# Kernel tuning notes

Hardware: AMD Instinct MI355X
Metric: run time of the kernel (lower is better)

## Reference

```python
import jax, jax.numpy as jnp
import numpy as np

J, H, MAXREL = 24, 8, 49  # num_joints, temporal heads, max_relative_position


def _pos_encoding(seq_len, d_model):
    pos = jnp.arange(seq_len, dtype=jnp.float32)[:, None]
    i = jnp.arange(d_model, dtype=jnp.float32)[None, :]
    angle = pos / jnp.power(10000.0, 2.0 * jnp.floor(i / 2.0) / d_model)
    return jnp.where(jnp.arange(d_model)[None, :] % 2 == 0, jnp.sin(angle), jnp.cos(angle))  # [S, D]


def _rel_index(seq_len):
    r = jnp.arange(seq_len)
    dist = jnp.clip(r[None, :] - r[:, None], -MAXREL, MAXREL) + MAXREL
    return dist  # [S, S] int


def setup_inputs() -> dict:
    key = jax.random.key(0)
    ks = jax.random.split(key, 12)
    B, S, D = 32, 120, 128
    depth = D // H
    s = 0.02
    x = jax.random.normal(ks[0], (B, S, J, D), dtype=jnp.float32)
    mask = jnp.triu(jnp.ones((1, 1, S, S), dtype=jnp.float32), k=1)  # look-ahead mask
    Wq = jax.random.normal(ks[1], (J, D, D), dtype=jnp.float32) * s
    bq = jnp.zeros((J, D), dtype=jnp.float32)
    Wk = jax.random.normal(ks[2], (J, D, D), dtype=jnp.float32) * s
    bk = jnp.zeros((J, D), dtype=jnp.float32)
    Wv = jax.random.normal(ks[3], (J, D, D), dtype=jnp.float32) * s
    bv = jnp.zeros((J, D), dtype=jnp.float32)
    Wo = jax.random.normal(ks[4], (D, D), dtype=jnp.float32) * s
    bo = jnp.zeros((D,), dtype=jnp.float32)
    key_table = jax.random.normal(ks[5], (2 * MAXREL + 1, depth), dtype=jnp.float32) * s
    val_table = jax.random.normal(ks[6], (2 * MAXREL + 1, depth), dtype=jnp.float32) * s
    return {"x": x, "mask": mask, "Wq": Wq, "bq": bq, "Wk": Wk, "bk": bk,
            "Wv": Wv, "bv": bv, "Wo": Wo, "bo": bo,
            "key_table": key_table, "val_table": val_table}


def reference(x, mask, Wq, bq, Wk, bk, Wv, bv, Wo, bo, key_table, val_table):
    B, S, _, D = x.shape
    depth = D // H
    # absolute positional encoding, broadcast over batch and joints
    x = x + _pos_encoding(S, D)[None, :, None, :]
    xj = jnp.transpose(x, (2, 0, 1, 3))  # [J, B, S, D]
    # per-joint linear projections (torch Linear: y = x @ W^T + b)
    q = jnp.einsum('jbsd,jed->jbse', xj, Wq) + bq[:, None, None, :]
    k = jnp.einsum('jbsd,jed->jbse', xj, Wk) + bk[:, None, None, :]
    v = jnp.einsum('jbsd,jed->jbse', xj, Wv) + bv[:, None, None, :]
    # split heads -> [J, B, H, S, depth]
    split = lambda t: t.reshape(J, B, S, H, depth).transpose(0, 1, 3, 2, 4)
    q, k, v = split(q), split(k), split(v)
    # relative key/value embeddings [S, S, depth]
    rel = _rel_index(S)
    rk = key_table[rel]
    rv = val_table[rel]
    logits = jnp.einsum('jbhsd,jbhtd->jbhst', q, k) + jnp.einsum('jbhsd,std->jbhst', q, rk)
    logits = logits / jnp.float32(np.sqrt(depth)) + mask * (-1e9)
    w = jax.nn.softmax(logits, axis=-1)  # [J, B, H, S, T]
    out = jnp.einsum('jbhst,jbhtd->jbhsd', w, v) + jnp.einsum('jbhst,std->jbhsd', w, rv)
    out = out.transpose(0, 1, 3, 2, 4).reshape(J, B, S, D)  # merge heads
    out = jnp.einsum('jbsd,ed->jbse', out, Wo) + bo  # shared output projection
    outputs = out.transpose(1, 2, 0, 3)  # [B, S, J, D]
    attn_weights = w[..., -1, :].transpose(1, 0, 2, 3)  # [B, J, H, T]
    return outputs, attn_weights
```

## Files before the change

kernel.cpp:

```cpp
#include <hip/hip_runtime.h>
#include <math.h>

#define Jn 24
#define Bn 32
#define Sn 120
#define Dn 128
#define Hn 8
#define DEP 16
#define ALD 136

#define QSCL 0.36067376022224085f

typedef short bf16x8 __attribute__((ext_vector_type(8)));
typedef float f32x4 __attribute__((ext_vector_type(4)));

#if __has_builtin(__builtin_amdgcn_exp2f)
#define EXP2(x) __builtin_amdgcn_exp2f(x)
#else
#define EXP2(x) exp2f(x)
#endif

__device__ __forceinline__ unsigned short f2b(float f) {
    union { float f; unsigned u; } v; v.f = f;
    unsigned r = v.u + 0x7FFFu + ((v.u >> 16) & 1u);
    return (unsigned short)(r >> 16);
}
__device__ __forceinline__ float b2f(unsigned u16) {
    union { unsigned u; float f; } v; v.u = u16 << 16;
    return v.f;
}

__global__ void pe_kernel(float* __restrict__ pe) {
    const int s = blockIdx.x, d = threadIdx.x;
    const float expo = (float)(2 * (d >> 1)) / (float)Dn;
    const float base = powf(10000.0f, -expo);
    const float ang = (float)s * base;
    pe[s * Dn + d] = (d & 1) ? cosf(ang) : sinf(ang);
}

__global__ __launch_bounds__(256)
void qkv_gemm(const float* __restrict__ x, const float* __restrict__ pe,
              const float* __restrict__ Wq, const float* __restrict__ bq,
              const float* __restrict__ Wk, const float* __restrict__ bk,
              const float* __restrict__ Wv, const float* __restrict__ bv,
              unsigned short* __restrict__ qg, unsigned short* __restrict__ kg,
              unsigned short* __restrict__ vg, int jbase)
{
    extern __shared__ unsigned short lsu[];
    unsigned short* As = lsu;
    unsigned short* Bs = lsu + 128 * ALD;

    const int bid = blockIdx.x;
    const int mt = bid % 30;
    const int jc = bid / 30;
    const int j = jbase + jc;
    const int tid = threadIdx.x;

    for (int idx = tid; idx < 128 * 32; idx += 256) {
        const int r = idx >> 5;
        const int c = (idx & 31) << 2;
        const int mflat = mt * 128 + r;
        const int b = mflat / Sn;
        const int s = mflat % Sn;
        const float4 xv = *(const float4*)(x + (((size_t)(b * Sn + s)) * Jn + j) * Dn + c);
        const float4 pv = *(const float4*)(pe + s * Dn + c);
        unsigned short* dst = As + r * ALD + c;
        dst[0] = f2b(xv.x + pv.x); dst[1] = f2b(xv.y + pv.y);
        dst[2] = f2b(xv.z + pv.z); dst[3] = f2b(xv.w + pv.w);
    }

    const int wid = tid >> 6;
    const int lane = tid & 63;
    const int wm = wid >> 1, wn = wid & 1;
    const int g = lane >> 4, q16 = lane & 15;

    for (int nt = 0; nt < 3; ++nt) {
        const float* Wsel = (nt == 0 ? Wq : (nt == 1 ? Wk : Wv)) + (size_t)j * Dn * Dn;
        const float* bsel = (nt == 0 ? bq : (nt == 1 ? bk : bv)) + (size_t)j * Dn;
        unsigned short* obuf = (nt == 0 ? qg : (nt == 1 ? kg : vg));
        const float scl = (nt == 0) ? QSCL : 1.0f;

        if (nt) __syncthreads();
        for (int idx = tid; idx < 128 * 32; idx += 256) {
            const int e = idx >> 5;
            const int c = (idx & 31) << 2;
            const float4 wv = *(const float4*)(Wsel + (size_t)e * Dn + c);
            unsigned short* dst = Bs + e * ALD + c;
            dst[0] = f2b(wv.x); dst[1] = f2b(wv.y); dst[2] = f2b(wv.z); dst[3] = f2b(wv.w);
        }
        __syncthreads();

        f32x4 acc[4][4];
        #pragma unroll
        for (int a = 0; a < 4; ++a)
            #pragma unroll
            for (int c2 = 0; c2 < 4; ++c2) acc[a][c2] = (f32x4){0.f, 0.f, 0.f, 0.f};

        #pragma unroll
        for (int ks = 0; ks < 4; ++ks) {
            const int kof = ks * 32 + g * 8;
            bf16x8 av[4], bvf[4];
            #pragma unroll
            for (int fr = 0; fr < 4; ++fr)
                av[fr] = *(const bf16x8*)(As + (wm * 64 + fr * 16 + q16) * ALD + kof);
            #pragma unroll
            for (int fc = 0; fc < 4; ++fc)
                bvf[fc] = *(const bf16x8*)(Bs + (wn * 64 + fc * 16 + q16) * ALD + kof);
            #pragma unroll
            for (int fr = 0; fr < 4; ++fr)
                #pragma unroll
                for (int fc = 0; fc < 4; ++fc)
                    acc[fr][fc] = __builtin_amdgcn_mfma_f32_16x16x32_bf16(av[fr], bvf[fc], acc[fr][fc], 0, 0, 0);
        }

        #pragma unroll
        for (int fc = 0; fc < 4; ++fc) {
            const int e = wn * 64 + fc * 16 + q16;
            const float be = bsel[e];
            const int h = e >> 4, ed = e & 15;
            #pragma unroll
            for (int fr = 0; fr < 4; ++fr) {
                #pragma unroll
                for (int r = 0; r < 4; ++r) {
                    const int mflat = mt * 128 + wm * 64 + fr * 16 + g * 4 + r;
                    const int b = mflat / Sn, s = mflat % Sn;
                    obuf[((size_t)((jc * Bn + b) * Hn + h)) * (Sn * DEP) + s * DEP + ed] =
                        f2b((acc[fr][fc][r] + be) * scl);
                }
            }
        }
    }
}

#define AB_LD  184
#define A_VCT  0
#define A_RKT  5888
#define A_RV0  8384
#define A_ABUF 8448
#define A_QRB  32000
#define A_BYTES 40448

__global__ __launch_bounds__(256)
void attn_mfma(const unsigned short* __restrict__ qg, const unsigned short* __restrict__ kg,
               const unsigned short* __restrict__ vg,
               const float* __restrict__ ktab, const float* __restrict__ vtab,
               unsigned short* __restrict__ out_pre, float* __restrict__ attn_w, int jbase)
{
    extern __shared__ char smc[];
    unsigned short* vct = (unsigned short*)(smc + A_VCT);
    unsigned short* rkt = (unsigned short*)(smc + A_RKT);
    float*          rv0 = (float*)(smc + A_RV0);

    const int tid = threadIdx.x;
    const int wid = tid >> 6;
    const int lane = tid & 63;
    const int l15 = lane & 15;
    const int g = lane >> 4;
    const int bh = blockIdx.x;
    const int jc = bh >> 8;
    const int b = (bh >> 3) & 31;
    const int h = bh & 7;
    const int j = jbase + jc;

    unsigned short* ab = (unsigned short*)(smc + A_ABUF) + wid * 16 * AB_LD;
    _Float16*      qrb = (_Float16*)(smc + A_QRB) + wid * 16 * 66;

    {
        unsigned* z = (unsigned*)smc;
        for (int idx = tid; idx < A_BYTES / 4; idx += 256) z[idx] = 0;
    }
    __syncthreads();
    const unsigned* vs = (const unsigned*)vg + (size_t)bh * 960;
    for (int idx = tid; idx < 960; idx += 256) {
        const int s = idx >> 3, ep = idx & 7;
        const unsigned u = vs[idx];
        vct[(2 * ep) * AB_LD + s] = (unsigned short)(u & 0xffffu);
        vct[(2 * ep + 1) * AB_LD + s] = (unsigned short)(u >> 16);
    }
    for (int idx = tid; idx < 800; idx += 256) {
        const int d = idx >> 4, e = idx & 15;
        vct[e * AB_LD + 120 + d] = f2b(vtab[d * DEP + e] - vtab[e]);
    }
    for (int idx = tid; idx < 800; idx += 256) {
        const int d = idx >> 4, e = idx & 15;
        rkt[d * 24 + e] = f2b(ktab[d * DEP + e]);
    }
    if (tid < 16) rv0[tid] = vtab[tid];
    __syncthreads();

    const unsigned short* qgu = qg + (size_t)bh * 1920;
    const unsigned short* kgu = kg + (size_t)bh * 1920;

    const bf16x8 zf = {0, 0, 0, 0, 0, 0, 0, 0};
    const f32x4 z4 = {0.f, 0.f, 0.f, 0.f};
    const float rv0f = rv0[l15];

    #pragma unroll
    for (int half = 0; half < 2; ++half) {
        const int m = half ? (7 - wid) : wid;

        const bf16x8 afr = (g < 2) ? *(const bf16x8*)(qgu + (16 * m + l15) * 16 + g * 8) : zf;
        f32x4 qr[4];
        #pragma unroll
        for (int n = 0; n < 4; ++n) {
            const bf16x8 bfr = (g < 2) ? *(const bf16x8*)(rkt + (16 * n + l15) * 24 + g * 8) : zf;
            qr[n] = __builtin_amdgcn_mfma_f32_16x16x32_bf16(afr, bfr, z4, 0, 0, 0);
        }
        f32x4 acc[8];
        #pragma unroll
        for (int n = 0; n < 8; ++n) {
            if (n > m) break;
            const bf16x8 bfr = (g < 2) ? *(const bf16x8*)(kgu + (16 * n + l15) * 16 + g * 8) : zf;
            acc[n] = __builtin_amdgcn_mfma_f32_16x16x32_bf16(afr, bfr, z4, 0, 0, 0);
        }
        #pragma unroll
        for (int n = 0; n < 4; ++n)
            #pragma unroll
            for (int r = 0; r < 4; ++r)
                qrb[(g * 4 + r) * 66 + 16 * n + l15] = (_Float16)qr[n][r];

        float rs[4];
        #pragma unroll
        for (int r = 0; r < 4; ++r) {
            const int srow = 16 * m + g * 4 + r;
            float pv[8];
            float tot = 0.f;
            #pragma unroll
            for (int n = 0; n < 8; ++n) {
                if (n > m) break;
                const int t = 16 * n + l15;
                const int dd = t - srow;
                int dist = dd + 49;
                dist = dist < 0 ? 0 : (dist > 49 ? 49 : dist);
                const float qrv = (float)qrb[(g * 4 + r) * 66 + dist];
                float p = 0.f;
                if (t <= srow) p = EXP2(acc[n][r] + qrv);
                pv[n] = p;
                tot += p;
            }
            #pragma unroll
            for (int mk = 1; mk < 16; mk <<= 1) tot += __shfl_xor(tot, mk);
            rs[r] = tot;
            #pragma unroll
            for (int n = 0; n < 8; ++n) {
                if (n > m) break;
                const int t = 16 * n + l15;
                const int dd = t - srow;
                const unsigned short pb = f2b(pv[n]);
                if (t < Sn)
                    ab[(g * 4 + r) * AB_LD + t] = pb;
                if (dd >= -48 && dd <= 0)
                    ab[(g * 4 + r) * AB_LD + dd + 169] = pb;
            }
            if (srow == Sn - 1) {
                const float inv = 1.f / tot;
                #pragma unroll
                for (int n = 0; n < 8; ++n) {
                    if (n > m) break;
                    const int t = 16 * n + l15;
                    if (t < Sn)
                        attn_w[(((size_t)(b * Jn + j)) * Hn + h) * Sn + t] = pv[n] * inv;
                }
            }
        }

        f32x4 oacc = z4;
        #pragma unroll
        for (int kt = 0; kt < 3; ++kt) {
            if (kt > (m >> 1)) break;
            const bf16x8 aw = *(const bf16x8*)(ab + l15 * AB_LD + kt * 32 + g * 8);
            const bf16x8 bv = *(const bf16x8*)(vct + l15 * AB_LD + kt * 32 + g * 8);
            oacc = __builtin_amdgcn_mfma_f32_16x16x32_bf16(aw, bv, oacc, 0, 0, 0);
        }
        #pragma unroll
        for (int kt = 3; kt < 5; ++kt) {
            const bf16x8 aw = *(const bf16x8*)(ab + l15 * AB_LD + kt * 32 + g * 8);
            const bf16x8 bv = *(const bf16x8*)(vct + l15 * AB_LD + kt * 32 + g * 8);
            oacc = __builtin_amdgcn_mfma_f32_16x16x32_bf16(aw, bv, oacc, 0, 0, 0);
        }
        {
            const bf16x8 aw = (g < 2) ? *(const bf16x8*)(ab + l15 * AB_LD + 160 + g * 8) : zf;
            const bf16x8 bv = (g < 2) ? *(const bf16x8*)(vct + l15 * AB_LD + 160 + g * 8) : zf;
            oacc = __builtin_amdgcn_mfma_f32_16x16x32_bf16(aw, bv, oacc, 0, 0, 0);
        }
        #pragma unroll
        for (int r = 0; r < 4; ++r) {
            const int srow = 16 * m + g * 4 + r;
            if (srow < Sn)
                out_pre[((size_t)((j * Bn + b) * Sn) + srow) * Dn + h * DEP + l15] =
                    f2b(oacc[r] / rs[r] + rv0f);
        }
    }
}

__global__ __launch_bounds__(256)
void oproj_gemm(const unsigned short* __restrict__ Ain, const float* __restrict__ Wo,
                const float* __restrict__ bo, float* __restrict__ out)
{
    extern __shared__ unsigned short lsu[];
    unsigned short* As = lsu;
    unsigned short* Bs = lsu + 128 * ALD;
    const int tid = threadIdx.x;
    const int mt = blockIdx.x;

    for (int idx = tid; idx < 128 * 16; idx += 256) {
        const int r = idx >> 4;
        const int c = (idx & 15) << 3;
        *(uint4*)(As + r * ALD + c) = *(const uint4*)(Ain + ((size_t)(mt * 128 + r)) * Dn + c);
    }
    for (int idx = tid; idx < 128 * 32; idx += 256) {
        const int e = idx >> 5;
        const int c = (idx & 31) << 2;
        const float4 wv = *(const float4*)(Wo + (size_t)e * Dn + c);
        unsigned short* dst = Bs + e * ALD + c;
        dst[0] = f2b(wv.x); dst[1] = f2b(wv.y); dst[2] = f2b(wv.z); dst[3] = f2b(wv.w);
    }
    __syncthreads();

    const int wid = tid >> 6;
    const int lane = tid & 63;
    const int wm = wid >> 1, wn = wid & 1;
    const int g = lane >> 4, q16 = lane & 15;

    f32x4 acc[4][4];
    #pragma unroll
    for (int a = 0; a < 4; ++a)
        #pragma unroll
        for (int c2 = 0; c2 < 4; ++c2) acc[a][c2] = (f32x4){0.f, 0.f, 0.f, 0.f};

    #pragma unroll
    for (int ks = 0; ks < 4; ++ks) {
        const int kof = ks * 32 + g * 8;
        bf16x8 av[4], bvf[4];
        #pragma unroll
        for (int fr = 0; fr < 4; ++fr)
            av[fr] = *(const bf16x8*)(As + (wm * 64 + fr * 16 + q16) * ALD + kof);
        #pragma unroll
        for (int fc = 0; fc < 4; ++fc)
            bvf[fc] = *(const bf16x8*)(Bs + (wn * 64 + fc * 16 + q16) * ALD + kof);
        #pragma unroll
        for (int fr = 0; fr < 4; ++fr)
            #pragma unroll
            for (int fc = 0; fc < 4; ++fc)
                acc[fr][fc] = __builtin_amdgcn_mfma_f32_16x16x32_bf16(av[fr], bvf[fc], acc[fr][fc], 0, 0, 0);
    }

    #pragma unroll
    for (int fc = 0; fc < 4; ++fc) {
        const int e = wn * 64 + fc * 16 + q16;
        const float be = bo[e];
        #pragma unroll
        for (int fr = 0; fr < 4; ++fr) {
            #pragma unroll
            for (int r = 0; r < 4; ++r) {
                const int m = mt * 128 + wm * 64 + fr * 16 + g * 4 + r;
                const int jj = m / (Bn * Sn);
                const int rem = m % (Bn * Sn);
                const int bb = rem / Sn, ss = rem % Sn;
                out[((size_t)(bb * Sn + ss) * Jn + jj) * Dn + e] = acc[fr][fc][r] + be;
            }
        }
    }
}

extern "C" void kernel_launch(void* const* d_in, const int* in_sizes, int n_in,
                              void* d_out, int out_size, void* d_ws, size_t ws_size,
                              hipStream_t stream)
{
    const float* x    = (const float*)d_in[0];
    const float* Wq   = (const float*)d_in[2];
    const float* bq   = (const float*)d_in[3];
    const float* Wk   = (const float*)d_in[4];
    const float* bk   = (const float*)d_in[5];
    const float* Wv   = (const float*)d_in[6];
    const float* bv   = (const float*)d_in[7];
    const float* Wo   = (const float*)d_in[8];
    const float* bo   = (const float*)d_in[9];
    const float* ktab = (const float*)d_in[10];
    const float* vtab = (const float*)d_in[11];

    float* out    = (float*)d_out;
    float* attn_w = out + (size_t)Bn * Sn * Jn * Dn;

    const size_t fullE = (size_t)Jn * Bn * Sn * Dn;
    int JCr = 24;
    {
        const size_t need = 65536 + 2 * (3 * fullE + fullE);
        if (ws_size < need) JCr = 6;
    }
    const size_t csz = (size_t)JCr * Bn * Hn * Sn * DEP;

    float* pe = (float*)d_ws;
    char* base = (char*)d_ws;
    unsigned short* qg = (unsigned short*)(base + 65536);
    unsigned short* kg = qg + csz;
    unsigned short* vg = kg + csz;
    unsigned short* out_pre = vg + csz;

    pe_kernel<<<Sn, Dn, 0, stream>>>(pe);
    const int gemm_lds = 2 * 128 * ALD * 2;
    for (int c = 0; c < Jn; c += JCr) {
        qkv_gemm<<<JCr * 30, 256, gemm_lds, stream>>>(
            x, pe, Wq, bq, Wk, bk, Wv, bv, qg, kg, vg, c);
        attn_mfma<<<JCr * Bn * Hn, 256, A_BYTES, stream>>>(
            qg, kg, vg, ktab, vtab, out_pre, attn_w, c);
    }
    oproj_gemm<<<(Jn * Bn * Sn) / 128, 256, gemm_lds, stream>>>(out_pre, Wo, bo, out);
}
```

Baseline: 225.8 us.

## Use hardware packed bf16 convert and simplify softmax relative-position indexing

Replaces the manual round-to-nearest bf16 conversion with the v_cvt_pk_bf16_f32 instruction and packs pairs of values into 32-bit LDS stores in the GEMM staging loops. The attention softmax loop is restructured: far tiles use a constant clipped relative-key term, the clamp logic is specialised per tile, and the probability store is folded into the exp loop. Divisions are replaced with hardware reciprocal plus fma, the qr LDS stride shrinks, and launch bounds request 4 blocks per CU. These changes cut ALU and LDS-store instruction count, at the cost of a slightly less exact reciprocal and more branchy code.

```diff
diff --git a/kernel.cpp b/kernel.cpp
--- a/kernel.cpp
+++ b/kernel.cpp
@@ -20,10 +20,13 @@
 #define EXP2(x) exp2f(x)
 #endif
 
-__device__ __forceinline__ unsigned short f2b(float f) {
-    union { float f; unsigned u; } v; v.f = f;
-    unsigned r = v.u + 0x7FFFu + ((v.u >> 16) & 1u);
-    return (unsigned short)(r >> 16);
+__device__ __forceinline__ unsigned f2b2(float a, float b) {
+    unsigned r;
+    asm("v_cvt_pk_bf16_f32 %0, %1, %2" : "=v"(r) : "v"(a), "v"(b));
+    return r;
+}
+__device__ __forceinline__ unsigned short f2bu(float f) {
+    return (unsigned short)f2b2(f, f);
 }
 __device__ __forceinline__ float b2f(unsigned u16) {
     union { unsigned u; float f; } v; v.u = u16 << 16;
@@ -64,9 +67,9 @@
         const int s = mflat % Sn;
         const float4 xv = *(const float4*)(x + (((size_t)(b * Sn + s)) * Jn + j) * Dn + c);
         const float4 pv = *(const float4*)(pe + s * Dn + c);
-        unsigned short* dst = As + r * ALD + c;
-        dst[0] = f2b(xv.x + pv.x); dst[1] = f2b(xv.y + pv.y);
-        dst[2] = f2b(xv.z + pv.z); dst[3] = f2b(xv.w + pv.w);
+        const unsigned lo = f2b2(xv.x + pv.x, xv.y + pv.y);
+        const unsigned hi = f2b2(xv.z + pv.z, xv.w + pv.w);
+        *(uint2*)(As + r * ALD + c) = make_uint2(lo, hi);
     }
 
     const int wid = tid >> 6;
@@ -85,8 +88,9 @@
             const int e = idx >> 5;
             const int c = (idx & 31) << 2;
             const float4 wv = *(const float4*)(Wsel + (size_t)e * Dn + c);
-            unsigned short* dst = Bs + e * ALD + c;
-            dst[0] = f2b(wv.x); dst[1] = f2b(wv.y); dst[2] = f2b(wv.z); dst[3] = f2b(wv.w);
+            const unsigned lo = f2b2(wv.x, wv.y);
+            const unsigned hi = f2b2(wv.z, wv.w);
+            *(uint2*)(Bs + e * ALD + c) = make_uint2(lo, hi);
         }
         __syncthreads();
 
@@ -125,7 +129,7 @@
                     const int mflat = mt * 128 + wm * 64 + fr * 16 + g * 4 + r;
                     const int b = mflat / Sn, s = mflat % Sn;
                     obuf[((size_t)((jc * Bn + b) * Hn + h)) * (Sn * DEP) + s * DEP + ed] =
-                        f2b((acc[fr][fc][r] + be) * scl);
+                        f2bu((acc[fr][fc][r] + be) * scl);
                 }
             }
         }
@@ -133,14 +137,15 @@
 }
 
 #define AB_LD  184
+#define QR_LD  52
 #define A_VCT  0
 #define A_RKT  5888
-#define A_RV0  8384
-#define A_ABUF 8448
-#define A_QRB  32000
-#define A_BYTES 40448
-
-__global__ __launch_bounds__(256)
+#define A_RV0  8960
+#define A_ABUF 9024
+#define A_QRB  32576
+#define A_BYTES 39264
+
+__global__ __launch_bounds__(256, 4)
 void attn_mfma(const unsigned short* __restrict__ qg, const unsigned short* __restrict__ kg,
                const unsigned short* __restrict__ vg,
                const float* __restrict__ ktab, const float* __restrict__ vtab,
@@ -163,7 +168,7 @@
     const int j = jbase + jc;
 
     unsigned short* ab = (unsigned short*)(smc + A_ABUF) + wid * 16 * AB_LD;
-    _Float16*      qrb = (_Float16*)(smc + A_QRB) + wid * 16 * 66;
+    _Float16*      qrb = (_Float16*)(smc + A_QRB) + wid * 16 * QR_LD;
 
     {
         unsigned* z = (unsigned*)smc;
@@ -179,11 +184,11 @@
     }
     for (int idx = tid; idx < 800; idx += 256) {
         const int d = idx >> 4, e = idx & 15;
-        vct[e * AB_LD + 120 + d] = f2b(vtab[d * DEP + e] - vtab[e]);
+        vct[e * AB_LD + 120 + d] = f2bu(vtab[d * DEP + e] - vtab[e]);
     }
     for (int idx = tid; idx < 800; idx += 256) {
         const int d = idx >> 4, e = idx & 15;
-        rkt[d * 24 + e] = f2b(ktab[d * DEP + e]);
+        rkt[d * 24 + e] = f2bu(ktab[d * DEP + e]);
     }
     if (tid < 16) rv0[tid] = vtab[tid];
     __syncthreads();
@@ -217,43 +222,53 @@
         for (int n = 0; n < 4; ++n)
             #pragma unroll
             for (int r = 0; r < 4; ++r)
-                qrb[(g * 4 + r) * 66 + 16 * n + l15] = (_Float16)qr[n][r];
+                if (n < 3 || l15 < 4)
+                    qrb[(g * 4 + r) * QR_LD + 16 * n + l15] = (_Float16)qr[n][r];
 
         float rs[4];
         #pragma unroll
         for (int r = 0; r < 4; ++r) {
-            const int srow = 16 * m + g * 4 + r;
+            const int row = g * 4 + r;
+            const int srow = 16 * m + row;
+            const int rowbase = row * AB_LD;
+            const _Float16* qrow = qrb + row * QR_LD;
+            const float qr0 = (float)qrow[0];
             float pv[8];
             float tot = 0.f;
             #pragma unroll
             for (int n = 0; n < 8; ++n) {
                 if (n > m) break;
-                const int t = 16 * n + l15;
-                const int dd = t - srow;
-                int dist = dd + 49;
-                dist = dist < 0 ? 0 : (dist > 49 ? 49 : dist);
-                const float qrv = (float)qrb[(g * 4 + r) * 66 + dist];
-                float p = 0.f;
-                if (t <= srow) p = EXP2(acc[n][r] + qrv);
+                float p;
+                if (n <= m - 4) {
+                    p = EXP2(acc[n][r] + qr0);
+                } else if (n < m) {
+                    int dist = 16 * (n - m) + 49 + l15 - row;
+                    if (n == m - 3) dist = dist < 0 ? 0 : dist;
+                    p = EXP2(acc[n][r] + (float)qrow[dist]);
+                } else {
+                    const int dist = 49 + l15 - row;
+                    p = (l15 <= row) ? EXP2(acc[n][r] + (float)qrow[dist]) : 0.f;
+                }
                 pv[n] = p;
                 tot += p;
+                if (n < 7 || l15 < 8)
+                    ab[rowbase + 16 * n + l15] = f2bu(p);
             }
             #pragma unroll
             for (int mk = 1; mk < 16; mk <<= 1) tot += __shfl_xor(tot, mk);
             rs[r] = tot;
+
             #pragma unroll
             for (int n = 0; n < 8; ++n) {
-                if (n > m) break;
-                const int t = 16 * n + l15;
-                const int dd = t - srow;
-                const unsigned short pb = f2b(pv[n]);
-                if (t < Sn)
-                    ab[(g * 4 + r) * AB_LD + t] = pb;
-                if (dd >= -48 && dd <= 0)
-                    ab[(g * 4 + r) * AB_LD + dd + 169] = pb;
+                if (n < m - 3 || n > m) continue;
+                const int dist = 16 * (n - m) + 49 + l15 - row;
+                bool st = true;
+                if (n == m - 3) st = (dist >= 1);
+                if (n == m)     st = (l15 <= row);
+                if (st) ab[rowbase + 120 + dist] = f2bu(pv[n]);
             }
             if (srow == Sn - 1) {
-                const float inv = 1.f / tot;
+                const float inv = __builtin_amdgcn_rcpf(tot);
                 #pragma unroll
                 for (int n = 0; n < 8; ++n) {
                     if (n > m) break;
@@ -286,9 +301,11 @@
         #pragma unroll
         for (int r = 0; r < 4; ++r) {
             const int srow = 16 * m + g * 4 + r;
-            if (srow < Sn)
+            if (srow < Sn) {
+                const float inv = __builtin_amdgcn_rcpf(rs[r]);
                 out_pre[((size_t)((j * Bn + b) * Sn) + srow) * Dn + h * DEP + l15] =
-                    f2b(oacc[r] / rs[r] + rv0f);
+                    f2bu(fmaf(oacc[r], inv, rv0f));
+            }
         }
     }
 }
@@ -312,8 +329,9 @@
         const int e = idx >> 5;
         const int c = (idx & 31) << 2;
         const float4 wv = *(const float4*)(Wo + (size_t)e * Dn + c);
-        unsigned short* dst = Bs + e * ALD + c;
-        dst[0] = f2b(wv.x); dst[1] = f2b(wv.y); dst[2] = f2b(wv.z); dst[3] = f2b(wv.w);
+        const unsigned lo = f2b2(wv.x, wv.y);
+        const unsigned hi = f2b2(wv.z, wv.w);
+        *(uint2*)(Bs + e * ALD + c) = make_uint2(lo, hi);
     }
     __syncthreads();
 
```

Result: slower. 271.6 us (+20.3%).
